# Optimization experiments

Measured on AMD Instinct MI355X. Metric: run time of the kernel, lower is better.

## Reference

```python
import jax, jax.numpy as jnp
import numpy as np

EMBED_DIM = 768
NUM_HEADS = 12
HEAD_DIM = EMBED_DIM // NUM_HEADS


def setup_inputs() -> dict:
    key = jax.random.key(0)
    k1, k2, k3, k4, k5 = jax.random.split(key, 5)
    x = jax.random.normal(k1, (2, 4096, EMBED_DIM), dtype=jnp.float32)
    # nn.Linear(embedding_dim, 3*embedding_dim): weight [3d, d], bias [3d]
    w_qkv = jax.random.normal(k2, (3 * EMBED_DIM, EMBED_DIM), dtype=jnp.float32) * (1.0 / np.sqrt(EMBED_DIM))
    b_qkv = jax.random.normal(k3, (3 * EMBED_DIM,), dtype=jnp.float32) * 0.02
    # LayerNorm affine params
    ln_gamma = jnp.ones((EMBED_DIM,), dtype=jnp.float32)
    ln_beta = jnp.zeros((EMBED_DIM,), dtype=jnp.float32)
    return {"x": x, "w_qkv": w_qkv, "b_qkv": b_qkv, "ln_gamma": ln_gamma, "ln_beta": ln_beta}


def _layernorm(x, gamma, beta, eps=1e-5):
    mu = jnp.mean(x, axis=-1, keepdims=True)
    var = jnp.var(x, axis=-1, keepdims=True)
    return (x - mu) * jax.lax.rsqrt(var + eps) * gamma + beta


def reference(x, w_qkv, b_qkv, ln_gamma, ln_beta):
    b, n, d = x.shape
    h, hd = NUM_HEADS, HEAD_DIM
    qkv = x @ w_qkv.T + b_qkv                      # [b, n, 3d]
    qkv = qkv.reshape(b, n, 3, h, hd)
    qkv = jnp.transpose(qkv, (2, 0, 3, 1, 4))      # [3, b, h, n, hd]
    Q, K, V = qkv[0], qkv[1], qkv[2]
    scale = 1.0 / np.sqrt(hd).astype(np.float32)
    scores = jnp.einsum('bhqd,bhkd->bhqk', Q, K) * scale   # [b, h, n, n]
    attn = jax.nn.softmax(scores, axis=-1)
    out = jnp.einsum('bhqk,bhkd->bhqd', attn, V)           # [b, h, n, hd]
    out = jnp.transpose(out, (0, 2, 1, 3)).reshape(b, n, d)
    return _layernorm(x + out, ln_gamma, ln_beta)
```

## Files before the change

### kernel.cpp

```cpp
#include <hip/hip_runtime.h>
#include <stdint.h>

#define NUM_HEADS 12
#define HEAD_DIM 64
#define EMB 768
#define SEQ 4096
#define BATCH 2
#define ROWS (BATCH*SEQ)
#define DQKV (3*EMB)

typedef __attribute__((ext_vector_type(8))) __bf16 bf16x8;
typedef __attribute__((ext_vector_type(4))) float floatx4;

static __device__ __forceinline__ unsigned short f2bf(float f) {
  unsigned int u = __float_as_uint(f);
  u += 0x7FFFu + ((u >> 16) & 1u);
  return (unsigned short)(u >> 16);
}

static __device__ __forceinline__ float bf2f(unsigned short h) {
  return __uint_as_float(((unsigned int)h) << 16);
}

static __device__ __forceinline__ unsigned int pack_bf2_trunc(float a, float b) {
  return __builtin_amdgcn_perm(__float_as_uint(b), __float_as_uint(a), 0x07060302u);
}

static __device__ __forceinline__ void async_cp16(void* lds, const void* g) {
  __builtin_amdgcn_global_load_lds(
      (__attribute__((address_space(1))) void*)(g),
      (__attribute__((address_space(3))) void*)(lds), 16, 0, 0);
}

static __device__ __forceinline__ int perm_key(int nn) {
  return (nn & ~31) | (((nn >> 2) & 3) * 8 + ((nn >> 4) & 1) * 4 + (nn & 3));
}

#define N4X (ROWS*EMB/4)
#define N4W (DQKV*EMB/4)
__global__ __launch_bounds__(256) void cvt2_kernel(
    const float* __restrict__ x, const float* __restrict__ w,
    unsigned short* __restrict__ xb, unsigned short* __restrict__ wb) {
  int i = blockIdx.x * blockDim.x + threadIdx.x;
  const float4* src;
  ushort4* dst;
  if (i < N4X) { src = (const float4*)x; dst = (ushort4*)xb; }
  else { i -= N4X; if (i >= N4W) return; src = (const float4*)w; dst = (ushort4*)wb; }
  float4 v = src[i];
  ushort4 o;
  o.x = f2bf(v.x); o.y = f2bf(v.y); o.z = f2bf(v.z); o.w = f2bf(v.w);
  dst[i] = o;
}

__global__ __launch_bounds__(256) void qkv_gemm_kernel(
    const unsigned short* __restrict__ xb, const unsigned short* __restrict__ wb,
    const float* __restrict__ bias,
    unsigned short* __restrict__ Qb, unsigned short* __restrict__ Kb,
    unsigned short* __restrict__ Vt) {
  __shared__ unsigned short As[128 * 64];
  __shared__ unsigned short Bs[128 * 64];
  const int t = threadIdx.x;
  const int lane = t & 63;
  const int w = t >> 6;
  const int wm = w >> 1, wn = w & 1;
  const int fr = lane & 15, fq = lane >> 4;
  const int fx = fr & 7;
  const int m0 = blockIdx.x * 128;
  const int n0 = blockIdx.y * 128;
  const int sel = n0 / EMB;
  const int lr = t >> 3;
  const int sc = t & 7;

  floatx4 acc[4][4];
#pragma unroll
  for (int i = 0; i < 4; ++i)
#pragma unroll
    for (int j = 0; j < 4; ++j) acc[i][j] = (floatx4)(0.0f);

  if (sel < 2) {
    for (int k0 = 0; k0 < EMB; k0 += 64) {
      __syncthreads();
#pragma unroll
      for (int i = 0; i < 4; ++i) {
        const int rr = i*32 + lr;
        const int cg = ((sc ^ (lr & 7)) * 8);
        async_cp16(&As[rr*64 + sc*8], &xb[(size_t)(m0 + rr)*EMB + k0 + cg]);
        async_cp16(&Bs[rr*64 + sc*8], &wb[(size_t)(n0 + rr)*EMB + k0 + cg]);
      }
      __syncthreads();
#pragma unroll
      for (int ks = 0; ks < 2; ++ks) {
        bf16x8 af[4], bfr[4];
#pragma unroll
        for (int i = 0; i < 4; ++i)
          af[i] = *(const bf16x8*)&As[(wm*64 + i*16 + fr)*64 + (((ks*4+fq) ^ fx)*8)];
#pragma unroll
        for (int j = 0; j < 4; ++j)
          bfr[j] = *(const bf16x8*)&Bs[(wn*64 + j*16 + fr)*64 + (((ks*4+fq) ^ fx)*8)];
#pragma unroll
        for (int i = 0; i < 4; ++i)
#pragma unroll
          for (int j = 0; j < 4; ++j)
            acc[i][j] = __builtin_amdgcn_mfma_f32_16x16x32_bf16(bfr[j], af[i], acc[i][j], 0, 0, 0);
      }
    }
    const float qscale = 0.125f * 1.4426950408889634f;
    const float sc2 = (sel == 0) ? qscale : 1.0f;
    unsigned short* dst = (sel == 0) ? Qb : Kb;
#pragma unroll
    for (int i = 0; i < 4; ++i) {
      const int mr = m0 + wm*64 + i*16 + fr;
      const int b = mr / SEQ;
      const int nn = mr - b*SEQ;
#pragma unroll
      for (int j = 0; j < 4; ++j) {
        const int og = n0 + wn*64 + j*16 + fq*4;
        const int oo = og - sel*EMB;
        const int hh = oo >> 6, dd = oo & 63;
        const float4 bv = *(const float4*)&bias[og];
        ushort4 pk;
        pk.x = f2bf((acc[i][j][0] + bv.x) * sc2);
        pk.y = f2bf((acc[i][j][1] + bv.y) * sc2);
        pk.z = f2bf((acc[i][j][2] + bv.z) * sc2);
        pk.w = f2bf((acc[i][j][3] + bv.w) * sc2);
        *(ushort4*)&dst[(((size_t)(b*NUM_HEADS + hh))*SEQ + nn)*HEAD_DIM + dd] = pk;
      }
    }
  } else {
    for (int k0 = 0; k0 < EMB; k0 += 64) {
      __syncthreads();
#pragma unroll
      for (int i = 0; i < 4; ++i) {
        const int rr = i*32 + lr;
        const int cg = ((sc ^ (lr & 7)) * 8);
        async_cp16(&As[rr*64 + sc*8], &xb[(size_t)(m0 + rr)*EMB + k0 + cg]);
        async_cp16(&Bs[rr*64 + sc*8], &wb[(size_t)(n0 + rr)*EMB + k0 + cg]);
      }
      __syncthreads();
#pragma unroll
      for (int ks = 0; ks < 2; ++ks) {
        bf16x8 af[4], bfr[4];
#pragma unroll
        for (int i = 0; i < 4; ++i)
          af[i] = *(const bf16x8*)&As[(wm*64 + i*16 + fr)*64 + (((ks*4+fq) ^ fx)*8)];
#pragma unroll
        for (int j = 0; j < 4; ++j)
          bfr[j] = *(const bf16x8*)&Bs[(wn*64 + j*16 + fr)*64 + (((ks*4+fq) ^ fx)*8)];
#pragma unroll
        for (int i = 0; i < 4; ++i)
#pragma unroll
          for (int j = 0; j < 4; ++j)
            acc[i][j] = __builtin_amdgcn_mfma_f32_16x16x32_bf16(af[i], bfr[j], acc[i][j], 0, 0, 0);
      }
    }
#pragma unroll
    for (int i = 0; i < 4; ++i) {
      const int mr = m0 + wm*64 + i*16 + fq*4;
      const int b = mr / SEQ;
      const int nn = perm_key(mr - b*SEQ);
#pragma unroll
      for (int j = 0; j < 4; ++j) {
        const int feat = n0 + wn*64 + j*16 + fr;
        const int oo = feat - 2*EMB;
        const int hh = oo >> 6, dd = oo & 63;
        const float bv = bias[feat];
        ushort4 pk;
        pk.x = f2bf(acc[i][j][0] + bv);
        pk.y = f2bf(acc[i][j][1] + bv);
        pk.z = f2bf(acc[i][j][2] + bv);
        pk.w = f2bf(acc[i][j][3] + bv);
        *(ushort4*)&Vt[(((size_t)(b*NUM_HEADS + hh))*HEAD_DIM + dd)*SEQ + nn] = pk;
      }
    }
  }
}

#define NT (SEQ/64)
__global__ __launch_bounds__(128, 2) void attn_kernel(
    const unsigned short* __restrict__ Qb, const unsigned short* __restrict__ Kb,
    const unsigned short* __restrict__ Vt, unsigned short* __restrict__ Oo) {
  __shared__ unsigned short Ks[2][64 * 64];
  __shared__ unsigned short Vs[2][64 * 64];
  const int t = threadIdx.x;
  const int lane = t & 63;
  const int w = t >> 6;
  const int fr = lane & 15, fq = lane >> 4;
  const int fx = fr & 7;
  const int bh = blockIdx.y;
  const int q0 = blockIdx.x * 128 + w * 64;

  bf16x8 aq[4][2];
#pragma unroll
  for (int g = 0; g < 4; ++g) {
    const size_t qoff = ((size_t)bh * SEQ + q0 + g*16 + fr) * HEAD_DIM;
    aq[g][0] = *(const bf16x8*)&Qb[qoff + fq*8];
    aq[g][1] = *(const bf16x8*)&Qb[qoff + 32 + fq*8];
  }

  union { unsigned int u[4]; bf16x8 b; } onesu;
  onesu.u[0] = onesu.u[1] = onesu.u[2] = onesu.u[3] = 0x3F803F80u;
  const bf16x8 onesb = onesu.b;

  floatx4 o[4][4];
  floatx4 lsum[4];
#pragma unroll
  for (int g = 0; g < 4; ++g) {
    lsum[g] = (floatx4)(0.f);
#pragma unroll
    for (int d = 0; d < 4; ++d) o[g][d] = (floatx4)(0.f);
  }

  const size_t kb = (size_t)bh * SEQ * HEAD_DIM;
  const size_t vb = (size_t)bh * HEAD_DIM * SEQ;

  auto stage = [&](int kc, int bi) {
#pragma unroll
    for (int i = 0; i < 4; ++i) {
      const int chunk = i*128 + t;
      const int r = chunk >> 3, c = chunk & 7;
      async_cp16(&Ks[bi][chunk*8], &Kb[kb + (size_t)(kc + r)*HEAD_DIM + ((c ^ (r&7))*8)]);
    }
#pragma unroll
    for (int i = 0; i < 4; ++i) {
      const int chunk = i*128 + t;
      const int r = chunk >> 3, c = chunk & 7;
      async_cp16(&Vs[bi][chunk*8], &Vt[vb + (size_t)r*SEQ + kc + ((c ^ (r&7))*8)]);
    }
  };

  auto chunk_compute = [&](const unsigned short* ksp, const unsigned short* vsp,
                           int J) {
    floatx4 z[4][2];
#pragma unroll
    for (int jj = 0; jj < 2; ++jj) {
      const int row = (J*2 + jj)*16 + fr;
      bf16x8 k0 = *(const bf16x8*)&ksp[row*64 + ((fq ^ fx)*8)];
      bf16x8 k1 = *(const bf16x8*)&ksp[row*64 + (((fq+4) ^ fx)*8)];
#pragma unroll
      for (int g = 0; g < 4; ++g) {
        floatx4 a = (floatx4)(0.f);
        a = __builtin_amdgcn_mfma_f32_16x16x32_bf16(k0, aq[g][0], a, 0, 0, 0);
        a = __builtin_amdgcn_mfma_f32_16x16x32_bf16(k1, aq[g][1], a, 0, 0, 0);
        z[g][jj] = a;
      }
    }
    bf16x8 vvb[4];
    const int vc = ((4*J + fq) ^ fx) * 8;
#pragma unroll
    for (int dt = 0; dt < 4; ++dt)
      vvb[dt] = *(const bf16x8*)&vsp[(dt*16 + fr)*64 + vc];
#pragma unroll
    for (int g = 0; g < 4; ++g) {
      float e0 = __builtin_amdgcn_exp2f(z[g][0][0]);
      float e1 = __builtin_amdgcn_exp2f(z[g][0][1]);
      float e2 = __builtin_amdgcn_exp2f(z[g][0][2]);
      float e3 = __builtin_amdgcn_exp2f(z[g][0][3]);
      float e4 = __builtin_amdgcn_exp2f(z[g][1][0]);
      float e5 = __builtin_amdgcn_exp2f(z[g][1][1]);
      float e6 = __builtin_amdgcn_exp2f(z[g][1][2]);
      float e7 = __builtin_amdgcn_exp2f(z[g][1][3]);
      union { unsigned int u[4]; bf16x8 b; } cv;
      cv.u[0] = pack_bf2_trunc(e0, e1);
      cv.u[1] = pack_bf2_trunc(e2, e3);
      cv.u[2] = pack_bf2_trunc(e4, e5);
      cv.u[3] = pack_bf2_trunc(e6, e7);
      const bf16x8 ap = cv.b;
      __builtin_amdgcn_s_setprio(1);
      lsum[g] = __builtin_amdgcn_mfma_f32_16x16x32_bf16(ap, onesb, lsum[g], 0, 0, 0);
#pragma unroll
      for (int dt = 0; dt < 4; ++dt)
        o[g][dt] = __builtin_amdgcn_mfma_f32_16x16x32_bf16(ap, vvb[dt], o[g][dt], 0, 0, 0);
      __builtin_amdgcn_s_setprio(0);
    }
  };

  stage(0, 0);
  stage(64, 1);
  asm volatile("s_waitcnt vmcnt(8)" ::: "memory");
  __builtin_amdgcn_s_barrier();

  int cur = 0;
  for (int tt = 0; tt < NT; ++tt) {
    const unsigned short* ksp = Ks[cur];
    const unsigned short* vsp = Vs[cur];
    chunk_compute(ksp, vsp, 0);
    chunk_compute(ksp, vsp, 1);
    if (tt == NT - 1) break;
    __builtin_amdgcn_s_barrier();
    if (tt + 2 < NT) {
      stage((tt + 2) * 64, cur);
      asm volatile("s_waitcnt vmcnt(8)" ::: "memory");
    } else {
      asm volatile("s_waitcnt vmcnt(0)" ::: "memory");
    }
    __builtin_amdgcn_s_barrier();
    cur ^= 1;
  }

  const int b = bh / NUM_HEADS, hh = bh - b*NUM_HEADS;
#pragma unroll
  for (int g = 0; g < 4; ++g)
#pragma unroll
    for (int r4 = 0; r4 < 4; ++r4) {
      const float li = 1.0f / lsum[g][r4];
      const size_t obase = ((size_t)b*SEQ + q0 + g*16 + fq*4 + r4)*EMB + hh*HEAD_DIM;
#pragma unroll
      for (int dt = 0; dt < 4; ++dt)
        Oo[obase + dt*16 + fr] = f2bf(o[g][dt][r4] * li);
    }
}

__global__ __launch_bounds__(256) void ln_kernel(
    const float* __restrict__ x, const unsigned short* __restrict__ att,
    const float* __restrict__ gamma, const float* __restrict__ beta,
    float* __restrict__ out) {
  const int row = blockIdx.x * 4 + (threadIdx.x >> 6);
  const int lane = threadIdx.x & 63;
  const size_t base = (size_t)row * EMB;
  float4 v[3];
  float s = 0.f, s2 = 0.f;
#pragma unroll
  for (int k = 0; k < 3; ++k) {
    const int c = lane*4 + k*256;
    const float4 xv = *(const float4*)&x[base + c];
    const ushort4 a4 = *(const ushort4*)&att[base + c];
    v[k].x = xv.x + bf2f(a4.x);
    v[k].y = xv.y + bf2f(a4.y);
    v[k].z = xv.z + bf2f(a4.z);
    v[k].w = xv.w + bf2f(a4.w);
    s  += (v[k].x + v[k].y) + (v[k].z + v[k].w);
    s2 += (v[k].x*v[k].x + v[k].y*v[k].y) + (v[k].z*v[k].z + v[k].w*v[k].w);
  }
#pragma unroll
  for (int off = 1; off < 64; off <<= 1) {
    s  += __shfl_xor(s,  off);
    s2 += __shfl_xor(s2, off);
  }
  const float mean = s * (1.0f / EMB);
  const float var  = s2 * (1.0f / EMB) - mean * mean;
  const float rstd = rsqrtf(var + 1e-5f);
#pragma unroll
  for (int k = 0; k < 3; ++k) {
    const int c = lane*4 + k*256;
    const float4 g4 = *(const float4*)&gamma[c];
    const float4 b4 = *(const float4*)&beta[c];
    float4 ov;
    ov.x = (v[k].x - mean) * rstd * g4.x + b4.x;
    ov.y = (v[k].y - mean) * rstd * g4.y + b4.y;
    ov.z = (v[k].z - mean) * rstd * g4.z + b4.z;
    ov.w = (v[k].w - mean) * rstd * g4.w + b4.w;
    *(float4*)&out[base + c] = ov;
  }
}

extern "C" void kernel_launch(void* const* d_in, const int* in_sizes, int n_in,
                              void* d_out, int out_size, void* d_ws, size_t ws_size,
                              hipStream_t stream) {
  const float* x      = (const float*)d_in[0];
  const float* w_qkv  = (const float*)d_in[1];
  const float* b_qkv  = (const float*)d_in[2];
  const float* gamma  = (const float*)d_in[3];
  const float* beta   = (const float*)d_in[4];
  float* out = (float*)d_out;

  unsigned short* xb = (unsigned short*)d_ws;
  unsigned short* wb = xb + (size_t)ROWS * EMB;
  unsigned short* Qb = wb + (size_t)DQKV * EMB;
  unsigned short* Kb = Qb + (size_t)ROWS * EMB;
  unsigned short* Vt = Kb + (size_t)ROWS * EMB;
  unsigned short* att = Vt + (size_t)ROWS * EMB;

  cvt2_kernel<<<(N4X + N4W + 255)/256, 256, 0, stream>>>(x, w_qkv, xb, wb);
  qkv_gemm_kernel<<<dim3(ROWS/128, DQKV/128), 256, 0, stream>>>(xb, wb, b_qkv, Qb, Kb, Vt);
  attn_kernel<<<dim3(SEQ/128, BATCH*NUM_HEADS), 128, 0, stream>>>(Qb, Kb, Vt, att);
  ln_kernel<<<ROWS/4, 256, 0, stream>>>(x, att, gamma, beta, out);
}
```

Measured before the change: 268.4 us.

## Split attention KV range in two and merge partials in layernorm

Adds a grid z-dimension so each attention block processes only half of the key/value sequence. Each block writes unnormalized fp32 partial outputs and row sums, and the layernorm kernel adds the two halves and normalizes. The aim is to double the block count and fix wave-quantization imbalance in the attention launch. The cost is larger fp32 partial buffers written and read back through global memory. The merge is only correct if both halves share the same softmax offset rather than a per-half running max.

```diff
diff --git a/kernel.cpp b/kernel.cpp
--- a/kernel.cpp
+++ b/kernel.cpp
@@ -175,10 +175,12 @@
   }
 }
 
-#define NT (SEQ/64)
+#define NKH (SEQ/2)
+#define NTH (NKH/64)
 __global__ __launch_bounds__(128, 2) void attn_kernel(
     const unsigned short* __restrict__ Qb, const unsigned short* __restrict__ Kb,
-    const unsigned short* __restrict__ Vt, unsigned short* __restrict__ Oo) {
+    const unsigned short* __restrict__ Vt,
+    float* __restrict__ Opart, float* __restrict__ lpart) {
   __shared__ unsigned short Ks[2][64 * 64];
   __shared__ unsigned short Vs[2][64 * 64];
   const int t = threadIdx.x;
@@ -187,6 +189,8 @@
   const int fr = lane & 15, fq = lane >> 4;
   const int fx = fr & 7;
   const int bh = blockIdx.y;
+  const int half = blockIdx.z;
+  const int kc0 = half * NKH;
   const int q0 = blockIdx.x * 128 + w * 64;
 
   bf16x8 aq[4][2];
@@ -274,21 +278,21 @@
     }
   };
 
-  stage(0, 0);
-  stage(64, 1);
+  stage(kc0, 0);
+  stage(kc0 + 64, 1);
   asm volatile("s_waitcnt vmcnt(8)" ::: "memory");
   __builtin_amdgcn_s_barrier();
 
   int cur = 0;
-  for (int tt = 0; tt < NT; ++tt) {
+  for (int tt = 0; tt < NTH; ++tt) {
     const unsigned short* ksp = Ks[cur];
     const unsigned short* vsp = Vs[cur];
     chunk_compute(ksp, vsp, 0);
     chunk_compute(ksp, vsp, 1);
-    if (tt == NT - 1) break;
+    if (tt == NTH - 1) break;
     __builtin_amdgcn_s_barrier();
-    if (tt + 2 < NT) {
-      stage((tt + 2) * 64, cur);
+    if (tt + 2 < NTH) {
+      stage(kc0 + (tt + 2) * 64, cur);
       asm volatile("s_waitcnt vmcnt(8)" ::: "memory");
     } else {
       asm volatile("s_waitcnt vmcnt(0)" ::: "memory");
@@ -297,37 +301,51 @@
     cur ^= 1;
   }
 
-  const int b = bh / NUM_HEADS, hh = bh - b*NUM_HEADS;
-#pragma unroll
-  for (int g = 0; g < 4; ++g)
+  const size_t pb = (size_t)(half * BATCH * NUM_HEADS + bh);
+  const size_t obase = pb * SEQ * HEAD_DIM;
+  const size_t lbase = pb * SEQ;
+#pragma unroll
+  for (int g = 0; g < 4; ++g) {
 #pragma unroll
     for (int r4 = 0; r4 < 4; ++r4) {
-      const float li = 1.0f / lsum[g][r4];
-      const size_t obase = ((size_t)b*SEQ + q0 + g*16 + fq*4 + r4)*EMB + hh*HEAD_DIM;
+      const int q = q0 + g*16 + fq*4 + r4;
+      float* op = &Opart[obase + (size_t)q * HEAD_DIM];
 #pragma unroll
       for (int dt = 0; dt < 4; ++dt)
-        Oo[obase + dt*16 + fr] = f2bf(o[g][dt][r4] * li);
-    }
+        op[dt*16 + fr] = o[g][dt][r4];
+      if (fr == 0) lpart[lbase + q] = lsum[g][r4];
+    }
+  }
 }
 
 __global__ __launch_bounds__(256) void ln_kernel(
-    const float* __restrict__ x, const unsigned short* __restrict__ att,
+    const float* __restrict__ x,
+    const float* __restrict__ Opart, const float* __restrict__ lpart,
     const float* __restrict__ gamma, const float* __restrict__ beta,
     float* __restrict__ out) {
   const int row = blockIdx.x * 4 + (threadIdx.x >> 6);
   const int lane = threadIdx.x & 63;
+  const int b = row >> 12;
+  const int n = row & (SEQ - 1);
   const size_t base = (size_t)row * EMB;
+  const size_t HSTRIDE = (size_t)BATCH * NUM_HEADS * SEQ;
+  const size_t HOSTRIDE = HSTRIDE * HEAD_DIM;
   float4 v[3];
   float s = 0.f, s2 = 0.f;
 #pragma unroll
   for (int k = 0; k < 3; ++k) {
     const int c = lane*4 + k*256;
+    const int h = c >> 6, d4 = c & 63;
+    const size_t oi = (((size_t)(b*NUM_HEADS + h))*SEQ + n)*HEAD_DIM + d4;
+    const size_t li = ((size_t)(b*NUM_HEADS + h))*SEQ + n;
+    const float4 p0 = *(const float4*)&Opart[oi];
+    const float4 p1 = *(const float4*)&Opart[oi + HOSTRIDE];
+    const float rl = 1.0f / (lpart[li] + lpart[li + HSTRIDE]);
     const float4 xv = *(const float4*)&x[base + c];
-    const ushort4 a4 = *(const ushort4*)&att[base + c];
-    v[k].x = xv.x + bf2f(a4.x);
-    v[k].y = xv.y + bf2f(a4.y);
-    v[k].z = xv.z + bf2f(a4.z);
-    v[k].w = xv.w + bf2f(a4.w);
+    v[k].x = xv.x + (p0.x + p1.x) * rl;
+    v[k].y = xv.y + (p0.y + p1.y) * rl;
+    v[k].z = xv.z + (p0.z + p1.z) * rl;
+    v[k].w = xv.w + (p0.w + p1.w) * rl;
     s  += (v[k].x + v[k].y) + (v[k].z + v[k].w);
     s2 += (v[k].x*v[k].x + v[k].y*v[k].y) + (v[k].z*v[k].z + v[k].w*v[k].w);
   }
@@ -368,10 +386,11 @@
   unsigned short* Qb = wb + (size_t)DQKV * EMB;
   unsigned short* Kb = Qb + (size_t)ROWS * EMB;
   unsigned short* Vt = Kb + (size_t)ROWS * EMB;
-  unsigned short* att = Vt + (size_t)ROWS * EMB;
+  float* Opart = (float*)(Vt + (size_t)ROWS * EMB);
+  float* lpart = Opart + (size_t)2 * ROWS * EMB;
 
   cvt2_kernel<<<(N4X + N4W + 255)/256, 256, 0, stream>>>(x, w_qkv, xb, wb);
   qkv_gemm_kernel<<<dim3(ROWS/128, DQKV/128), 256, 0, stream>>>(xb, wb, b_qkv, Qb, Kb, Vt);
-  attn_kernel<<<dim3(SEQ/128, BATCH*NUM_HEADS), 128, 0, stream>>>(Qb, Kb, Vt, att);
-  ln_kernel<<<ROWS/4, 256, 0, stream>>>(x, att, gamma, beta, out);
-}
+  attn_kernel<<<dim3(SEQ/128, BATCH*NUM_HEADS, 2), 128, 0, stream>>>(Qb, Kb, Vt, Opart, lpart);
+  ln_kernel<<<ROWS/4, 256, 0, stream>>>(x, Opart, lpart, gamma, beta, out);
+}
```

Measured after the change: 278.5 us. 1.04x slower.
